# Optimization experiments

Measured on AMD Instinct MI355X. Metric: run time of the kernel, lower is better.

Reference implementation:

```python
import jax, jax.numpy as jnp
import numpy as np

N_NODES = 50000
N_EDGES = 800000
IN_DIM = 64
OUT_DIM = 64
N_GRAPHS = 64
EPS = 1e-16  # PyG softmax eps


def setup_inputs() -> dict:
    key = jax.random.key(0)
    ks = jax.random.split(key, 12)
    x = jax.random.normal(ks[0], (N_NODES, IN_DIM), dtype=jnp.float32)
    edge_index = jax.random.randint(ks[1], (2, N_EDGES), 0, N_NODES, dtype=jnp.int64)
    batch = jnp.sort(jax.random.randint(ks[2], (N_NODES,), 0, N_GRAPHS, dtype=jnp.int64))
    s = 1.0 / np.sqrt(IN_DIM)
    Wq = jax.random.normal(ks[3], (IN_DIM, OUT_DIM), dtype=jnp.float32) * s
    bq = jnp.zeros((OUT_DIM,), dtype=jnp.float32)
    Wk = jax.random.normal(ks[4], (IN_DIM, OUT_DIM), dtype=jnp.float32) * s
    bk = jnp.zeros((OUT_DIM,), dtype=jnp.float32)
    Wv = jax.random.normal(ks[5], (IN_DIM, OUT_DIM), dtype=jnp.float32) * s
    bv = jnp.zeros((OUT_DIM,), dtype=jnp.float32)
    Wskip = jax.random.normal(ks[6], (IN_DIM, OUT_DIM), dtype=jnp.float32) * s
    bskip = jnp.zeros((OUT_DIM,), dtype=jnp.float32)
    return {"x": x, "edge_index": edge_index, "batch": batch,
            "Wq": Wq, "bq": bq, "Wk": Wk, "bk": bk, "Wv": Wv, "bv": bv,
            "Wskip": Wskip, "bskip": bskip}


def _global_encoder(x, edge_index, batch, Wq, bq, Wk, bk, Wv, bv, Wskip, bskip):
    src, dst = edge_index[0], edge_index[1]  # messages flow src -> dst
    q = x @ Wq + bq                          # [N, D]
    k = x @ Wk + bk
    v = x @ Wv + bv
    qi = q[dst]                              # [E, D] gather at target
    kj = k[src]                              # [E, D] gather at source
    vj = v[src]
    logits = jnp.sum(qi * kj, axis=-1) / jnp.sqrt(jnp.float32(OUT_DIM))  # [E]
    # segment softmax over incoming edges of each dst node
    m = jax.ops.segment_max(logits, dst, num_segments=N_NODES)           # [N]
    m = jnp.where(jnp.isfinite(m), m, 0.0)
    e = jnp.exp(logits - m[dst])                                         # [E]
    denom = jax.ops.segment_sum(e, dst, num_segments=N_NODES)            # [N]
    alpha = e / (denom[dst] + EPS)                                       # [E]
    agg = jax.ops.segment_sum(alpha[:, None] * vj, dst, num_segments=N_NODES)  # [N, D]
    out = agg + (x @ Wskip + bskip)          # root/skip connection
    out = jax.nn.relu(out)
    # global mean pool over graphs
    sums = jax.ops.segment_sum(out, batch, num_segments=N_GRAPHS)        # [B, D]
    cnt = jax.ops.segment_sum(jnp.ones((x.shape[0],), out.dtype), batch, num_segments=N_GRAPHS)
    return sums / jnp.maximum(cnt, 1.0)[:, None]


def reference(x, edge_index, batch, Wq, bq, Wk, bk, Wv, bv, Wskip, bskip):
    return _global_encoder(x, edge_index, batch, Wq, bq, Wk, bk, Wv, bv, Wskip, bskip)
```

## Files before the change

kernel.cpp:

```cpp
#include <hip/hip_runtime.h>

#define D64 64
#define EPS 1e-16f

__device__ __forceinline__ float dot4(float4 a, float4 b) {
    return a.x * b.x + a.y * b.y + a.z * b.z + a.w * b.w;
}
__device__ __forceinline__ float rsum16(float p) {
    p += __shfl_xor(p, 1);
    p += __shfl_xor(p, 2);
    p += __shfl_xor(p, 4);
    p += __shfl_xor(p, 8);
    return p;
}

__global__ __launch_bounds__(256) void qkvs_kernel(
    const float* __restrict__ x,
    const float* __restrict__ Wq, const float* __restrict__ bq,
    const float* __restrict__ Wk, const float* __restrict__ bk,
    const float* __restrict__ Wv, const float* __restrict__ bv,
    const float* __restrict__ Ws, const float* __restrict__ bs,
    float* __restrict__ q, float* __restrict__ k, float* __restrict__ v,
    float* __restrict__ skip, int n_nodes,
    const int* __restrict__ dst, int* __restrict__ deg, int E)
{
    __shared__ float wq[4096], wk[4096], wv[4096];
    __shared__ float xs[16 * 64];
    __shared__ float bqs[64], bks[64], bvs[64], bss[64];
    int t = threadIdx.x;
    for (int i = t; i < 1024; i += 256) {
        ((float4*)wq)[i] = ((const float4*)Wq)[i];
        ((float4*)wk)[i] = ((const float4*)Wk)[i];
        ((float4*)wv)[i] = ((const float4*)Wv)[i];
    }
    if (t < 64) { bqs[t] = bq[t]; bks[t] = bk[t]; bvs[t] = bv[t]; bss[t] = bs[t]; }
    __syncthreads();

    int d  = t & 63;
    int j0 = t >> 6;
    int ntiles = (n_nodes + 15) / 16;
    for (int tile = blockIdx.x; tile < ntiles; tile += gridDim.x) {
        int base = tile * 16;
        __syncthreads();
        if (base + 16 <= n_nodes) {
            ((float4*)xs)[t] = ((const float4*)x)[(size_t)base * 16 + t];
        } else {
            for (int i = t; i < 1024; i += 256) {
                int node = base + (i >> 6);
                xs[i] = (node < n_nodes) ? x[(size_t)node * 64 + (i & 63)] : 0.0f;
            }
        }
        __syncthreads();

        float aq[4], ak[4], av[4], asv[4];
        #pragma unroll
        for (int j = 0; j < 4; ++j) { aq[j] = bqs[d]; ak[j] = bks[d]; av[j] = bvs[d]; asv[j] = bss[d]; }
        #pragma unroll 8
        for (int i = 0; i < 64; ++i) {
            float w0 = wq[i * 64 + d];
            float w1 = wk[i * 64 + d];
            float w2 = wv[i * 64 + d];
            float w3 = Ws[i * 64 + d];
            #pragma unroll
            for (int j = 0; j < 4; ++j) {
                float xi = xs[(j0 * 4 + j) * 64 + i];
                aq[j]  += xi * w0;
                ak[j]  += xi * w1;
                av[j]  += xi * w2;
                asv[j] += xi * w3;
            }
        }
        #pragma unroll
        for (int j = 0; j < 4; ++j) {
            int node = base + j0 * 4 + j;
            if (node < n_nodes) {
                size_t o = (size_t)node * 64 + d;
                q[o] = aq[j]; k[o] = ak[j]; v[o] = av[j]; skip[o] = asv[j];
            }
        }
    }

    for (int e = blockIdx.x * 256 + t; e < E; e += gridDim.x * 256)
        atomicAdd(deg + dst[e], 1);
}

__global__ __launch_bounds__(1024) void scan_kernel(
    const int* __restrict__ deg, int* __restrict__ rowstart, int N, int E)
{
    __shared__ int sums[1024];
    int t = threadIdx.x;
    int chunk = (N + 1023) >> 10;
    int beg = t * chunk;
    int end = min(beg + chunk, N);
    int s = 0;
    for (int i = beg; i < end; ++i) s += deg[i];
    sums[t] = s;
    __syncthreads();
    for (int off = 1; off < 1024; off <<= 1) {
        int add = (t >= off) ? sums[t - off] : 0;
        __syncthreads();
        sums[t] += add;
        __syncthreads();
    }
    int prefix = (t == 0) ? 0 : sums[t - 1];
    for (int i = beg; i < end; ++i) { rowstart[i] = prefix; prefix += deg[i]; }
    if (t == 0) rowstart[N] = E;
}

__global__ __launch_bounds__(256) void fill_kernel(
    const int* __restrict__ src, const int* __restrict__ dst,
    const int* __restrict__ rowstart, int* __restrict__ cursor,
    int* __restrict__ srcs, int E)
{
    int e = blockIdx.x * 256 + threadIdx.x;
    if (e >= E) return;
    int d = dst[e];
    int pos = rowstart[d] + atomicAdd(cursor + d, 1);
    srcs[pos] = src[e];
}

__global__ __launch_bounds__(256) void attn_gather_kernel(
    const float* __restrict__ q, const float* __restrict__ k,
    const float* __restrict__ v, const float* __restrict__ skip,
    const int* __restrict__ rowstart, const int* __restrict__ srcs,
    const int* __restrict__ batch,
    float* __restrict__ out, float* __restrict__ cnt, int N)
{
    int t = threadIdx.x;
    int l = t & 15;
    int node = (blockIdx.x * 256 + t) >> 4;
    bool valid = node < N;

    float4 qv = make_float4(0.f, 0.f, 0.f, 0.f);
    int p0 = 0, p1 = 0;
    if (valid) {
        qv = ((const float4*)q)[(size_t)node * 16 + l];
        p0 = rowstart[node];
        p1 = rowstart[node + 1];
    }

    float4 acc = make_float4(0.f, 0.f, 0.f, 0.f);
    float den = 0.f;
    float m = -INFINITY;

    const float4* k4 = (const float4*)k;
    const float4* v4 = (const float4*)v;

    int p = p0;
    for (; p + 4 <= p1; p += 4) {
        int s0 = srcs[p + 0];
        int s1 = srcs[p + 1];
        int s2 = srcs[p + 2];
        int s3 = srcs[p + 3];
        float4 k0 = k4[(size_t)s0 * 16 + l];
        float4 k1 = k4[(size_t)s1 * 16 + l];
        float4 k2 = k4[(size_t)s2 * 16 + l];
        float4 k3 = k4[(size_t)s3 * 16 + l];
        float4 v0 = v4[(size_t)s0 * 16 + l];
        float4 v1 = v4[(size_t)s1 * 16 + l];
        float4 v2 = v4[(size_t)s2 * 16 + l];
        float4 v3 = v4[(size_t)s3 * 16 + l];

        float l0 = rsum16(dot4(qv, k0)) * 0.125f;
        float l1 = rsum16(dot4(qv, k1)) * 0.125f;
        float l2 = rsum16(dot4(qv, k2)) * 0.125f;
        float l3 = rsum16(dot4(qv, k3)) * 0.125f;

        float mx = fmaxf(fmaxf(l0, l1), fmaxf(l2, l3));
        if (mx > m) {
            float sc = __expf(m - mx);
            den *= sc;
            acc.x *= sc; acc.y *= sc; acc.z *= sc; acc.w *= sc;
            m = mx;
        }
        float e0 = __expf(l0 - m);
        float e1 = __expf(l1 - m);
        float e2 = __expf(l2 - m);
        float e3 = __expf(l3 - m);
        den += (e0 + e1) + (e2 + e3);
        acc.x += e0 * v0.x + e1 * v1.x + e2 * v2.x + e3 * v3.x;
        acc.y += e0 * v0.y + e1 * v1.y + e2 * v2.y + e3 * v3.y;
        acc.z += e0 * v0.z + e1 * v1.z + e2 * v2.z + e3 * v3.z;
        acc.w += e0 * v0.w + e1 * v1.w + e2 * v2.w + e3 * v3.w;
    }
    for (; p < p1; ++p) {
        int s = srcs[p];
        float4 kj = k4[(size_t)s * 16 + l];
        float4 vj = v4[(size_t)s * 16 + l];
        float logit = rsum16(dot4(qv, kj)) * 0.125f;
        if (logit > m) {
            float sc = __expf(m - logit);
            den *= sc;
            acc.x *= sc; acc.y *= sc; acc.z *= sc; acc.w *= sc;
            m = logit;
        }
        float ev = __expf(logit - m);
        den += ev;
        acc.x += ev * vj.x; acc.y += ev * vj.y;
        acc.z += ev * vj.z; acc.w += ev * vj.w;
    }

    float4 val = make_float4(0.f, 0.f, 0.f, 0.f);
    int g = -1;
    if (valid) {
        float inv = 1.0f / (den + EPS);
        float4 sk = ((const float4*)skip)[(size_t)node * 16 + l];
        val.x = fmaxf(acc.x * inv + sk.x, 0.f);
        val.y = fmaxf(acc.y * inv + sk.y, 0.f);
        val.z = fmaxf(acc.z * inv + sk.z, 0.f);
        val.w = fmaxf(acc.w * inv + sk.w, 0.f);
        g = batch[node];
    }

    int g0 = __shfl(g, 0);
    bool uni = __all(g == g0);
    if (uni) {
        if (g0 >= 0) {
            val.x += __shfl_xor(val.x, 16); val.x += __shfl_xor(val.x, 32);
            val.y += __shfl_xor(val.y, 16); val.y += __shfl_xor(val.y, 32);
            val.z += __shfl_xor(val.z, 16); val.z += __shfl_xor(val.z, 32);
            val.w += __shfl_xor(val.w, 16); val.w += __shfl_xor(val.w, 32);
            if ((t & 63) < 16) {
                float* o = out + (size_t)g0 * 64 + l * 4;
                atomicAdd(o + 0, val.x);
                atomicAdd(o + 1, val.y);
                atomicAdd(o + 2, val.z);
                atomicAdd(o + 3, val.w);
            }
            if ((t & 63) == 0) atomicAdd(cnt + g0, 4.0f);
        }
    } else if (valid) {
        float* o = out + (size_t)g * 64 + l * 4;
        atomicAdd(o + 0, val.x);
        atomicAdd(o + 1, val.y);
        atomicAdd(o + 2, val.z);
        atomicAdd(o + 3, val.w);
        if (l == 0) atomicAdd(cnt + g, 1.0f);
    }
}

__global__ __launch_bounds__(256) void pool_div_kernel(
    float* __restrict__ out, const float* __restrict__ cnt, int n)
{
    int idx = blockIdx.x * 256 + threadIdx.x;
    if (idx >= n) return;
    int g = idx >> 6;
    out[idx] /= fmaxf(cnt[g], 1.0f);
}

extern "C" void kernel_launch(void* const* d_in, const int* in_sizes, int n_in,
                              void* d_out, int out_size, void* d_ws, size_t ws_size,
                              hipStream_t stream) {
    const float* x     = (const float*)d_in[0];
    const int*   eidx  = (const int*)d_in[1];
    const int*   batch = (const int*)d_in[2];
    const float* Wq = (const float*)d_in[3];
    const float* bq = (const float*)d_in[4];
    const float* Wk = (const float*)d_in[5];
    const float* bk = (const float*)d_in[6];
    const float* Wv = (const float*)d_in[7];
    const float* bv = (const float*)d_in[8];
    const float* Ws = (const float*)d_in[9];
    const float* bs = (const float*)d_in[10];

    int N = in_sizes[0] / D64;
    int E = in_sizes[1] / 2;
    const int* src = eidx;
    const int* dst = eidx + E;

    char* w = (char*)d_ws;
    size_t NB = (size_t)N * D64 * sizeof(float);
    float* q    = (float*)(w);
    float* k    = (float*)(w + NB);
    float* v    = (float*)(w + 2 * NB);
    float* skip = (float*)(w + 3 * NB);
    char*  p    = w + 4 * NB;
    int*   deg      = (int*)p;                 p += (size_t)N * 4;
    int*   cursor   = (int*)p;                 p += (size_t)N * 4;
    int*   rowstart = (int*)p;                 p += (size_t)(N + 1) * 4;
    int*   srcs     = (int*)p;                 p += (size_t)E * 4;
    float* cnt      = (float*)p;

    hipMemsetAsync(deg, 0, 2 * (size_t)N * 4, stream);
    hipMemsetAsync(cnt, 0, 64 * sizeof(float), stream);
    hipMemsetAsync(d_out, 0, (size_t)out_size * sizeof(float), stream);

    qkvs_kernel<<<1024, 256, 0, stream>>>(x, Wq, bq, Wk, bk, Wv, bv, Ws, bs,
                                          q, k, v, skip, N, dst, deg, E);
    scan_kernel<<<1, 1024, 0, stream>>>(deg, rowstart, N, E);
    int blocks_e = (E + 255) / 256;
    fill_kernel<<<blocks_e, 256, 0, stream>>>(src, dst, rowstart, cursor, srcs, E);
    int blocks_g = ((size_t)N * 16 + 255) / 256;
    attn_gather_kernel<<<blocks_g, 256, 0, stream>>>(q, k, v, skip, rowstart, srcs,
                                                     batch, (float*)d_out, cnt, N);
    pool_div_kernel<<<(out_size + 255) / 256, 256, 0, stream>>>((float*)d_out,
                                                                (const float*)cnt, out_size);
}
```

Baseline: 385.0 us.

## Store K and V as interleaved bf16 rows to halve gather traffic

```diff
diff --git a/kernel.cpp b/kernel.cpp
--- a/kernel.cpp
+++ b/kernel.cpp
@@ -3,8 +3,15 @@
 #define D64 64
 #define EPS 1e-16f
 
-__device__ __forceinline__ float dot4(float4 a, float4 b) {
-    return a.x * b.x + a.y * b.y + a.z * b.z + a.w * b.w;
+typedef unsigned int uint;
+typedef uint uivec4 __attribute__((ext_vector_type(4)));
+
+__device__ __forceinline__ float bf_lo(uint u) { return __uint_as_float(u << 16); }
+__device__ __forceinline__ float bf_hi(uint u) { return __uint_as_float(u & 0xffff0000u); }
+__device__ __forceinline__ unsigned short f2bf(float f) {
+    uint u = __float_as_uint(f);
+    u += 0x7fffu + ((u >> 16) & 1u);
+    return (unsigned short)(u >> 16);
 }
 __device__ __forceinline__ float rsum16(float p) {
     p += __shfl_xor(p, 1);
@@ -14,13 +21,22 @@
     return p;
 }
 
+#define DEC8(V, h)                                              \
+    h[0] = bf_lo(V[0]); h[1] = bf_hi(V[0]);                     \
+    h[2] = bf_lo(V[1]); h[3] = bf_hi(V[1]);                     \
+    h[4] = bf_lo(V[2]); h[5] = bf_hi(V[2]);                     \
+    h[6] = bf_lo(V[3]); h[7] = bf_hi(V[3]);
+
+#define DOT8(a, b) (a[0]*b[0] + a[1]*b[1] + a[2]*b[2] + a[3]*b[3] + \
+                    a[4]*b[4] + a[5]*b[5] + a[6]*b[6] + a[7]*b[7])
+
 __global__ __launch_bounds__(256) void qkvs_kernel(
     const float* __restrict__ x,
     const float* __restrict__ Wq, const float* __restrict__ bq,
     const float* __restrict__ Wk, const float* __restrict__ bk,
     const float* __restrict__ Wv, const float* __restrict__ bv,
     const float* __restrict__ Ws, const float* __restrict__ bs,
-    float* __restrict__ q, float* __restrict__ k, float* __restrict__ v,
+    float* __restrict__ q, unsigned short* __restrict__ kv,
     float* __restrict__ skip, int n_nodes,
     const int* __restrict__ dst, int* __restrict__ deg, int E)
 {
@@ -75,7 +91,11 @@
             int node = base + j0 * 4 + j;
             if (node < n_nodes) {
                 size_t o = (size_t)node * 64 + d;
-                q[o] = aq[j]; k[o] = ak[j]; v[o] = av[j]; skip[o] = asv[j];
+                q[o] = aq[j];
+                skip[o] = asv[j];
+                unsigned short* row = kv + (size_t)node * 128;
+                row[d]      = f2bf(ak[j]);
+                row[64 + d] = f2bf(av[j]);
             }
         }
     }
@@ -120,8 +140,8 @@
 }
 
 __global__ __launch_bounds__(256) void attn_gather_kernel(
-    const float* __restrict__ q, const float* __restrict__ k,
-    const float* __restrict__ v, const float* __restrict__ skip,
+    const float* __restrict__ q, const uint* __restrict__ kv,
+    const float* __restrict__ skip,
     const int* __restrict__ rowstart, const int* __restrict__ srcs,
     const int* __restrict__ batch,
     float* __restrict__ out, float* __restrict__ cnt, int N)
@@ -131,20 +151,28 @@
     int node = (blockIdx.x * 256 + t) >> 4;
     bool valid = node < N;
 
-    float4 qv = make_float4(0.f, 0.f, 0.f, 0.f);
+    float q8[8];
+    #pragma unroll
+    for (int j = 0; j < 8; ++j) q8[j] = 0.f;
     int p0 = 0, p1 = 0;
     if (valid) {
-        qv = ((const float4*)q)[(size_t)node * 16 + l];
+        if (l < 8) {
+            float4 a = ((const float4*)q)[(size_t)node * 16 + l * 2 + 0];
+            float4 b = ((const float4*)q)[(size_t)node * 16 + l * 2 + 1];
+            q8[0] = a.x; q8[1] = a.y; q8[2] = a.z; q8[3] = a.w;
+            q8[4] = b.x; q8[5] = b.y; q8[6] = b.z; q8[7] = b.w;
+        }
         p0 = rowstart[node];
         p1 = rowstart[node + 1];
     }
 
-    float4 acc = make_float4(0.f, 0.f, 0.f, 0.f);
+    float acc[8];
+    #pragma unroll
+    for (int j = 0; j < 8; ++j) acc[j] = 0.f;
     float den = 0.f;
     float m = -INFINITY;
 
-    const float4* k4 = (const float4*)k;
-    const float4* v4 = (const float4*)v;
+    const uivec4* kv4 = (const uivec4*)kv;
 
     int p = p0;
     for (; p + 4 <= p1; p += 4) {
@@ -152,25 +180,24 @@
         int s1 = srcs[p + 1];
         int s2 = srcs[p + 2];
         int s3 = srcs[p + 3];
-        float4 k0 = k4[(size_t)s0 * 16 + l];
-        float4 k1 = k4[(size_t)s1 * 16 + l];
-        float4 k2 = k4[(size_t)s2 * 16 + l];
-        float4 k3 = k4[(size_t)s3 * 16 + l];
-        float4 v0 = v4[(size_t)s0 * 16 + l];
-        float4 v1 = v4[(size_t)s1 * 16 + l];
-        float4 v2 = v4[(size_t)s2 * 16 + l];
-        float4 v3 = v4[(size_t)s3 * 16 + l];
-
-        float l0 = rsum16(dot4(qv, k0)) * 0.125f;
-        float l1 = rsum16(dot4(qv, k1)) * 0.125f;
-        float l2 = rsum16(dot4(qv, k2)) * 0.125f;
-        float l3 = rsum16(dot4(qv, k3)) * 0.125f;
+        uivec4 w0 = kv4[(size_t)s0 * 16 + l];
+        uivec4 w1 = kv4[(size_t)s1 * 16 + l];
+        uivec4 w2 = kv4[(size_t)s2 * 16 + l];
+        uivec4 w3 = kv4[(size_t)s3 * 16 + l];
+        float h0[8], h1[8], h2[8], h3[8];
+        DEC8(w0, h0) DEC8(w1, h1) DEC8(w2, h2) DEC8(w3, h3)
+
+        float l0 = rsum16(DOT8(q8, h0)) * 0.125f;
+        float l1 = rsum16(DOT8(q8, h1)) * 0.125f;
+        float l2 = rsum16(DOT8(q8, h2)) * 0.125f;
+        float l3 = rsum16(DOT8(q8, h3)) * 0.125f;
 
         float mx = fmaxf(fmaxf(l0, l1), fmaxf(l2, l3));
         if (mx > m) {
             float sc = __expf(m - mx);
             den *= sc;
-            acc.x *= sc; acc.y *= sc; acc.z *= sc; acc.w *= sc;
+            #pragma unroll
+            for (int j = 0; j < 8; ++j) acc[j] *= sc;
             m = mx;
         }
         float e0 = __expf(l0 - m);
@@ -178,37 +205,47 @@
         float e2 = __expf(l2 - m);
         float e3 = __expf(l3 - m);
         den += (e0 + e1) + (e2 + e3);
-        acc.x += e0 * v0.x + e1 * v1.x + e2 * v2.x + e3 * v3.x;
-        acc.y += e0 * v0.y + e1 * v1.y + e2 * v2.y + e3 * v3.y;
-        acc.z += e0 * v0.z + e1 * v1.z + e2 * v2.z + e3 * v3.z;
-        acc.w += e0 * v0.w + e1 * v1.w + e2 * v2.w + e3 * v3.w;
+        #pragma unroll
+        for (int j = 0; j < 8; ++j)
+            acc[j] += e0 * h0[j] + e1 * h1[j] + e2 * h2[j] + e3 * h3[j];
     }
     for (; p < p1; ++p) {
         int s = srcs[p];
-        float4 kj = k4[(size_t)s * 16 + l];
-        float4 vj = v4[(size_t)s * 16 + l];
-        float logit = rsum16(dot4(qv, kj)) * 0.125f;
-        if (logit > m) {
-            float sc = __expf(m - logit);
+        uivec4 w0 = kv4[(size_t)s * 16 + l];
+        float h0[8];
+        DEC8(w0, h0)
+        float lg = rsum16(DOT8(q8, h0)) * 0.125f;
+        if (lg > m) {
+            float sc = __expf(m - lg);
             den *= sc;
-            acc.x *= sc; acc.y *= sc; acc.z *= sc; acc.w *= sc;
-            m = logit;
-        }
-        float ev = __expf(logit - m);
+            #pragma unroll
+            for (int j = 0; j < 8; ++j) acc[j] *= sc;
+            m = lg;
+        }
+        float ev = __expf(lg - m);
         den += ev;
-        acc.x += ev * vj.x; acc.y += ev * vj.y;
-        acc.z += ev * vj.z; acc.w += ev * vj.w;
-    }
-
-    float4 val = make_float4(0.f, 0.f, 0.f, 0.f);
+        #pragma unroll
+        for (int j = 0; j < 8; ++j) acc[j] += ev * h0[j];
+    }
+
+    float o8[8];
+    #pragma unroll
+    for (int j = 0; j < 8; ++j) o8[j] = 0.f;
     int g = -1;
     if (valid) {
-        float inv = 1.0f / (den + EPS);
-        float4 sk = ((const float4*)skip)[(size_t)node * 16 + l];
-        val.x = fmaxf(acc.x * inv + sk.x, 0.f);
-        val.y = fmaxf(acc.y * inv + sk.y, 0.f);
-        val.z = fmaxf(acc.z * inv + sk.z, 0.f);
-        val.w = fmaxf(acc.w * inv + sk.w, 0.f);
+        if (l >= 8) {
+            float inv = 1.0f / (den + EPS);
+            float4 sa = ((const float4*)skip)[(size_t)node * 16 + (l - 8) * 2 + 0];
+            float4 sb = ((const float4*)skip)[(size_t)node * 16 + (l - 8) * 2 + 1];
+            o8[0] = fmaxf(acc[0] * inv + sa.x, 0.f);
+            o8[1] = fmaxf(acc[1] * inv + sa.y, 0.f);
+            o8[2] = fmaxf(acc[2] * inv + sa.z, 0.f);
+            o8[3] = fmaxf(acc[3] * inv + sa.w, 0.f);
+            o8[4] = fmaxf(acc[4] * inv + sb.x, 0.f);
+            o8[5] = fmaxf(acc[5] * inv + sb.y, 0.f);
+            o8[6] = fmaxf(acc[6] * inv + sb.z, 0.f);
+            o8[7] = fmaxf(acc[7] * inv + sb.w, 0.f);
+        }
         g = batch[node];
     }
 
@@ -216,26 +253,24 @@
     bool uni = __all(g == g0);
     if (uni) {
         if (g0 >= 0) {
-            val.x += __shfl_xor(val.x, 16); val.x += __shfl_xor(val.x, 32);
-            val.y += __shfl_xor(val.y, 16); val.y += __shfl_xor(val.y, 32);
-            val.z += __shfl_xor(val.z, 16); val.z += __shfl_xor(val.z, 32);
-            val.w += __shfl_xor(val.w, 16); val.w += __shfl_xor(val.w, 32);
-            if ((t & 63) < 16) {
-                float* o = out + (size_t)g0 * 64 + l * 4;
-                atomicAdd(o + 0, val.x);
-                atomicAdd(o + 1, val.y);
-                atomicAdd(o + 2, val.z);
-                atomicAdd(o + 3, val.w);
-            }
-            if ((t & 63) == 0) atomicAdd(cnt + g0, 4.0f);
-        }
-    } else if (valid) {
-        float* o = out + (size_t)g * 64 + l * 4;
-        atomicAdd(o + 0, val.x);
-        atomicAdd(o + 1, val.y);
-        atomicAdd(o + 2, val.z);
-        atomicAdd(o + 3, val.w);
-        if (l == 0) atomicAdd(cnt + g, 1.0f);
+            #pragma unroll
+            for (int j = 0; j < 8; ++j) {
+                o8[j] += __shfl_xor(o8[j], 16);
+                o8[j] += __shfl_xor(o8[j], 32);
+            }
+            int wl = t & 63;
+            if (wl >= 8 && wl < 16) {
+                float* o = out + (size_t)g0 * 64 + (l - 8) * 8;
+                #pragma unroll
+                for (int j = 0; j < 8; ++j) atomicAdd(o + j, o8[j]);
+            }
+            if (wl == 0) atomicAdd(cnt + g0, 4.0f);
+        }
+    } else if (valid && l >= 8) {
+        float* o = out + (size_t)g * 64 + (l - 8) * 8;
+        #pragma unroll
+        for (int j = 0; j < 8; ++j) atomicAdd(o + j, o8[j]);
+        if (l == 8) atomicAdd(cnt + g, 1.0f);
     }
 }
 
@@ -270,29 +305,29 @@
 
     char* w = (char*)d_ws;
     size_t NB = (size_t)N * D64 * sizeof(float);
-    float* q    = (float*)(w);
-    float* k    = (float*)(w + NB);
-    float* v    = (float*)(w + 2 * NB);
-    float* skip = (float*)(w + 3 * NB);
-    char*  p    = w + 4 * NB;
+    float*          q    = (float*)(w);
+    float*          skip = (float*)(w + NB);
+    unsigned short* kv   = (unsigned short*)(w + 2 * NB);
+    char* p = w + 3 * NB;
     int*   deg      = (int*)p;                 p += (size_t)N * 4;
     int*   cursor   = (int*)p;                 p += (size_t)N * 4;
     int*   rowstart = (int*)p;                 p += (size_t)(N + 1) * 4;
     int*   srcs     = (int*)p;                 p += (size_t)E * 4;
     float* cnt      = (float*)p;
 
-    hipMemsetAsync(deg, 0, 2 * (size_t)N * 4, stream);
-    hipMemsetAsync(cnt, 0, 64 * sizeof(float), stream);
-    hipMemsetAsync(d_out, 0, (size_t)out_size * sizeof(float), stream);
+    (void)hipMemsetAsync(deg, 0, 2 * (size_t)N * 4, stream);
+    (void)hipMemsetAsync(cnt, 0, 64 * sizeof(float), stream);
+    (void)hipMemsetAsync(d_out, 0, (size_t)out_size * sizeof(float), stream);
 
     qkvs_kernel<<<1024, 256, 0, stream>>>(x, Wq, bq, Wk, bk, Wv, bv, Ws, bs,
-                                          q, k, v, skip, N, dst, deg, E);
+                                          q, kv, skip, N, dst, deg, E);
     scan_kernel<<<1, 1024, 0, stream>>>(deg, rowstart, N, E);
     int blocks_e = (E + 255) / 256;
     fill_kernel<<<blocks_e, 256, 0, stream>>>(src, dst, rowstart, cursor, srcs, E);
     int blocks_g = ((size_t)N * 16 + 255) / 256;
-    attn_gather_kernel<<<blocks_g, 256, 0, stream>>>(q, k, v, skip, rowstart, srcs,
-                                                     batch, (float*)d_out, cnt, N);
+    attn_gather_kernel<<<blocks_g, 256, 0, stream>>>(q, (const uint*)kv, skip,
+                                                     rowstart, srcs, batch,
+                                                     (float*)d_out, cnt, N);
     pool_div_kernel<<<(out_size + 255) / 256, 256, 0, stream>>>((float*)d_out,
                                                                 (const float*)cnt, out_size);
 }
```

Result: slower. 427.6 us (+11.1%).
